# Kernel optimization log

Hardware: AMD Instinct MI355X
Metric: run time of the kernel (lower is better)

## Reference

```python
import jax, jax.numpy as jnp
import numpy as np

K = 5          # kernel_size
PAD = (K - 1) // 2  # fixed_padding with dilation=1, stride=1 -> 'same'


def setup_inputs() -> dict:
    key = jax.random.key(0)
    kx, kw = jax.random.split(key)
    x = jax.random.normal(kx, (4, 8, 512, 512), dtype=jnp.float32)
    # nn.Parameter initialized to zeros in the original; use small random values
    # so the op is non-trivial (math is identical for any weight values).
    weight = jax.random.normal(kw, (8, 8, K, K), dtype=jnp.float32) * 0.05
    return {"x": x, "weight": weight}


def reference(x, weight):
    """Morphological dilation2d with hard max (soft_max=False).

    out[n,o,h,w] = max_{c,dy,dx} ( x_pad[n,c,h+dy,w+dx] + weight[o,c,dy,dx] )
    Faithful to: pad zeros -> unfold -> weight + x -> max over dim C*k*k.
    Computed as a fused sliding-window max-plus reduction (no (N,C,k,k,H,W)
    unfold tensor is materialized; loop is over the fixed k*k kernel taps).
    """
    N, C, H, W = x.shape
    O = weight.shape[0]
    xp = jnp.pad(x, ((0, 0), (0, 0), (PAD, PAD), (PAD, PAD)))  # zero pad, as in F.pad
    out = jnp.full((N, O, H, W), -jnp.inf, dtype=x.dtype)
    for dy in range(K):
        for dx in range(K):
            patch = xp[:, :, dy:dy + H, dx:dx + W]           # (N,C,H,W)
            w_tap = weight[:, :, dy, dx]                      # (O,C)
            # (N,1,C,H,W) + (1,O,C,1,1) -> max over C -> (N,O,H,W)
            term = patch[:, None] + w_tap[None, :, :, None, None]
            out = jnp.maximum(out, jnp.max(term, axis=2))
    return out
```

## Files before the change

### kernel.cpp

```cpp
#include <hip/hip_runtime.h>
#include <math.h>
#include <stdint.h>

#define KK 5
#define PADK 2
#define C_IN 8
#define O_OUT 8
#define HH 512
#define WW 512
#define TH 8
#define TW 128
#define CH 4
#define LROWS 12
#define LCOLS 136
#define WSTR 12
#define NW (O_OUT * C_IN * KK * KK)
#define XHALF (CH * LROWS * (LCOLS / 2))

static __device__ __forceinline__ float max3f(float a, float b, float c) {
    float d;
    asm("v_max3_f32 %0, %1, %2, %3" : "=v"(d) : "v"(a), "v"(b), "v"(c));
    return d;
}

__global__ __launch_bounds__(512, 8)
void dil_kernel(const float* __restrict__ x,
                const float* __restrict__ wf,
                float* __restrict__ out) {
    __shared__ __align__(16) float xlds[CH][LROWS][LCOLS];
    __shared__ __align__(16) float wlds[C_IN * 4 * KK * WSTR];

    const int tid = threadIdx.x;
    const int w0 = blockIdx.x * TW;
    const int h0 = blockIdx.y * TH;
    const int n  = blockIdx.z;
    const float* xn = x + (size_t)n * (C_IN * HH * WW);

    const int l   = tid & 63;
    const int wid = tid >> 6;
    const int og  = wid & 3;
    const int rq  = wid >> 2;
    const int rbase = rq * 4;

    float acc[2][4][2];
    #pragma unroll
    for (int a = 0; a < 2; ++a)
        #pragma unroll
        for (int j = 0; j < 4; ++j) {
            acc[a][j][0] = -INFINITY;
            acc[a][j][1] = -INFINITY;
        }

    for (int h = 0; h < 2; ++h) {
        if (h) __syncthreads();

        for (int idx = tid; idx < XHALF; idx += 512) {
            int cc  = idx / (LROWS * (LCOLS / 2));
            int rem = idx - cc * (LROWS * (LCOLS / 2));
            int r   = rem / (LCOLS / 2);
            int jp  = rem - r * (LCOLS / 2);
            int gh = h0 - PADK + r;
            int gw = w0 - PADK + 2 * jp;
            float v0 = 0.f, v1 = 0.f;
            if ((unsigned)gh < (unsigned)HH) {
                const float* row = xn + ((size_t)(h * CH + cc) * HH + gh) * WW;
                if ((unsigned)gw < (unsigned)WW) v0 = row[gw];
                if ((unsigned)(gw + 1) < (unsigned)WW) v1 = row[gw + 1];
            }
            *(float2*)&xlds[cc][r][2 * jp] = make_float2(v0, v1);
        }
        if (h == 0) {
            for (int t = tid; t < NW; t += 512) {
                int dx = t % KK;  int q = t / KK;
                int o2 = q & 1;   q >>= 1;
                int dy = q % KK;  q /= KK;
                int g  = q & 3;   int c = q >> 2;
                int o = g * 2 + o2;
                wlds[((c * 4 + g) * KK + dy) * WSTR + o2 * KK + dx] =
                    wf[((o * C_IN + c) * KK + dy) * KK + dx];
            }
        }
        __syncthreads();

        for (int cc = 0; cc < CH; ++cc) {
            const float* wb = &wlds[((h * CH + cc) * 4 + og) * KK * WSTR];
            #pragma unroll
            for (int dy = 0; dy < KK; ++dy) {
                const float* wch = wb + dy * WSTR;
                float4 wa = *(const float4*)(wch);
                float4 wv = *(const float4*)(wch + 4);
                float2 wc2 = *(const float2*)(wch + 8);
                const float w[10] = {wa.x, wa.y, wa.z, wa.w,
                                     wv.x, wv.y, wv.z, wv.w, wc2.x, wc2.y};
                #pragma unroll
                for (int j = 0; j < 4; ++j) {
                    const float* lr = &xlds[cc][rbase + dy + j][2 * l];
                    float2 a = *(const float2*)(lr);
                    float2 b = *(const float2*)(lr + 2);
                    float2 d = *(const float2*)(lr + 4);
                    const float u0 = a.x, u1 = a.y, u2 = b.x,
                                u3 = b.y, u4 = d.x, u5 = d.y;
                    #pragma unroll
                    for (int o2 = 0; o2 < 2; ++o2) {
                        const float* wo = &w[o2 * 5];
                        float t0 = u0 + wo[0], t1 = u1 + wo[1],
                              t2 = u2 + wo[2], t3 = u3 + wo[3],
                              t4 = u4 + wo[4];
                        acc[o2][j][0] = max3f(acc[o2][j][0],
                                              max3f(t0, t1, t2),
                                              fmaxf(t3, t4));
                        float s0 = u1 + wo[0], s1 = u2 + wo[1],
                              s2 = u3 + wo[2], s3 = u4 + wo[3],
                              s4 = u5 + wo[4];
                        acc[o2][j][1] = max3f(acc[o2][j][1],
                                              max3f(s0, s1, s2),
                                              fmaxf(s3, s4));
                    }
                }
            }
        }
    }

    float* onp = out + (size_t)n * (O_OUT * HH * WW);
    const int hB = h0 + rbase;
    const int wcol = w0 + 2 * l;
    #pragma unroll
    for (int o2 = 0; o2 < 2; ++o2) {
        const int o = og * 2 + o2;
        #pragma unroll
        for (int j = 0; j < 4; ++j) {
            float2 rr = make_float2(acc[o2][j][0], acc[o2][j][1]);
            *(float2*)(&onp[((size_t)o * HH + hB + j) * WW + wcol]) = rr;
        }
    }
}

extern "C" void kernel_launch(void* const* d_in, const int* in_sizes, int n_in,
                              void* d_out, int out_size, void* d_ws, size_t ws_size,
                              hipStream_t stream) {
    const float* x   = (const float*)d_in[0];
    const float* wgt = (const float*)d_in[1];
    float* out = (float*)d_out;

    dim3 grid(WW / TW, HH / TH, 4);
    dim3 block(512);
    dil_kernel<<<grid, block, 0, stream>>>(x, wgt, out);
}
```

Measured before the change: 66.59 us.

## Remap warps to one row each computing all eight output channels

Each wavefront now owns one output row and accumulates all eight output channels, where before it owned four rows for two channels. Each loaded x window is reused across eight channels instead of two, cutting LDS reads of x per result. Weight loads from LDS rise, since each thread reads weights for all four channel groups per dy, though these reads are broadcast. The weight layout in LDS is reordered to match the new loop order.

```diff
diff --git a/kernel.cpp b/kernel.cpp
--- a/kernel.cpp
+++ b/kernel.cpp
@@ -28,7 +28,7 @@
                 const float* __restrict__ wf,
                 float* __restrict__ out) {
     __shared__ __align__(16) float xlds[CH][LROWS][LCOLS];
-    __shared__ __align__(16) float wlds[C_IN * 4 * KK * WSTR];
+    __shared__ __align__(16) float wlds[C_IN * KK * 4 * WSTR];
 
     const int tid = threadIdx.x;
     const int w0 = blockIdx.x * TW;
@@ -38,18 +38,13 @@
 
     const int l   = tid & 63;
     const int wid = tid >> 6;
-    const int og  = wid & 3;
-    const int rq  = wid >> 2;
-    const int rbase = rq * 4;
 
-    float acc[2][4][2];
+    float acc[O_OUT][2];
     #pragma unroll
-    for (int a = 0; a < 2; ++a)
-        #pragma unroll
-        for (int j = 0; j < 4; ++j) {
-            acc[a][j][0] = -INFINITY;
-            acc[a][j][1] = -INFINITY;
-        }
+    for (int o = 0; o < O_OUT; ++o) {
+        acc[o][0] = -INFINITY;
+        acc[o][1] = -INFINITY;
+    }
 
     for (int h = 0; h < 2; ++h) {
         if (h) __syncthreads();
@@ -76,45 +71,48 @@
                 int dy = q % KK;  q /= KK;
                 int g  = q & 3;   int c = q >> 2;
                 int o = g * 2 + o2;
-                wlds[((c * 4 + g) * KK + dy) * WSTR + o2 * KK + dx] =
+                wlds[((c * KK + dy) * 4 + g) * WSTR + o2 * KK + dx] =
                     wf[((o * C_IN + c) * KK + dy) * KK + dx];
             }
         }
         __syncthreads();
 
         for (int cc = 0; cc < CH; ++cc) {
-            const float* wb = &wlds[((h * CH + cc) * 4 + og) * KK * WSTR];
+            const int c = h * CH + cc;
             #pragma unroll
             for (int dy = 0; dy < KK; ++dy) {
-                const float* wch = wb + dy * WSTR;
-                float4 wa = *(const float4*)(wch);
-                float4 wv = *(const float4*)(wch + 4);
-                float2 wc2 = *(const float2*)(wch + 8);
-                const float w[10] = {wa.x, wa.y, wa.z, wa.w,
-                                     wv.x, wv.y, wv.z, wv.w, wc2.x, wc2.y};
+                const float* lr = &xlds[cc][wid + dy][2 * l];
+                float2 a = *(const float2*)(lr);
+                float2 b = *(const float2*)(lr + 2);
+                float2 d = *(const float2*)(lr + 4);
+                const float u0 = a.x, u1 = a.y, u2 = b.x,
+                            u3 = b.y, u4 = d.x, u5 = d.y;
+                const float* wdy = &wlds[(c * KK + dy) * 4 * WSTR];
                 #pragma unroll
-                for (int j = 0; j < 4; ++j) {
-                    const float* lr = &xlds[cc][rbase + dy + j][2 * l];
-                    float2 a = *(const float2*)(lr);
-                    float2 b = *(const float2*)(lr + 2);
-                    float2 d = *(const float2*)(lr + 4);
-                    const float u0 = a.x, u1 = a.y, u2 = b.x,
-                                u3 = b.y, u4 = d.x, u5 = d.y;
+                for (int g = 0; g < 4; ++g) {
+                    const float* wch = wdy + g * WSTR;
+                    float4 wa = *(const float4*)(wch);
+                    float4 wv = *(const float4*)(wch + 4);
+                    float2 wc2 = *(const float2*)(wch + 8);
+                    const float w[10] = {wa.x, wa.y, wa.z, wa.w,
+                                         wv.x, wv.y, wv.z, wv.w,
+                                         wc2.x, wc2.y};
                     #pragma unroll
                     for (int o2 = 0; o2 < 2; ++o2) {
+                        const int o = g * 2 + o2;
                         const float* wo = &w[o2 * 5];
                         float t0 = u0 + wo[0], t1 = u1 + wo[1],
                               t2 = u2 + wo[2], t3 = u3 + wo[3],
                               t4 = u4 + wo[4];
-                        acc[o2][j][0] = max3f(acc[o2][j][0],
-                                              max3f(t0, t1, t2),
-                                              fmaxf(t3, t4));
+                        acc[o][0] = max3f(acc[o][0],
+                                          max3f(t0, t1, t2),
+                                          fmaxf(t3, t4));
                         float s0 = u1 + wo[0], s1 = u2 + wo[1],
                               s2 = u3 + wo[2], s3 = u4 + wo[3],
                               s4 = u5 + wo[4];
-                        acc[o2][j][1] = max3f(acc[o2][j][1],
-                                              max3f(s0, s1, s2),
-                                              fmaxf(s3, s4));
+                        acc[o][1] = max3f(acc[o][1],
+                                          max3f(s0, s1, s2),
+                                          fmaxf(s3, s4));
                     }
                 }
             }
@@ -122,16 +120,12 @@
     }
 
     float* onp = out + (size_t)n * (O_OUT * HH * WW);
-    const int hB = h0 + rbase;
+    const int hB = h0 + wid;
     const int wcol = w0 + 2 * l;
     #pragma unroll
-    for (int o2 = 0; o2 < 2; ++o2) {
-        const int o = og * 2 + o2;
-        #pragma unroll
-        for (int j = 0; j < 4; ++j) {
-            float2 rr = make_float2(acc[o2][j][0], acc[o2][j][1]);
-            *(float2*)(&onp[((size_t)o * HH + hB + j) * WW + wcol]) = rr;
-        }
+    for (int o = 0; o < O_OUT; ++o) {
+        float2 rr = make_float2(acc[o][0], acc[o][1]);
+        *(float2*)(&onp[((size_t)o * HH + hB) * WW + wcol]) = rr;
     }
 }
 
```

Result: no change. 67.54 us (+1.4%).

## Prefetch second channel half into registers while computing first half

Applied to the files above, without the earlier changes.

Global loads of the input tile are staged through registers. The second channel-half is issued before computing the first half, so its memory latency overlaps the max-plus compute. Loads become unconditional, clamped float2 reads, with zero padding applied at LDS write time, which removes the branchy scalar loads. The cost is 14 extra VGPRs per thread under launch bounds of 512 threads with a minimum of 8 blocks per multiprocessor, which may cause spills or reduce occupancy.

```diff
diff --git a/kernel.cpp b/kernel.cpp
--- a/kernel.cpp
+++ b/kernel.cpp
@@ -16,6 +16,7 @@
 #define WSTR 12
 #define NW (O_OUT * C_IN * KK * KK)
 #define XHALF (CH * LROWS * (LCOLS / 2))
+#define NSTG 7
 
 static __device__ __forceinline__ float max3f(float a, float b, float c) {
     float d;
@@ -39,8 +40,49 @@
     const int l   = tid & 63;
     const int wid = tid >> 6;
     const int og  = wid & 3;
-    const int rq  = wid >> 2;
-    const int rbase = rq * 4;
+    const int rbase = (wid >> 2) * 4;
+
+    float2 stg[NSTG];
+
+    auto stageL = [&](int h) {
+        #pragma unroll
+        for (int k = 0; k < NSTG; ++k) {
+            int idx = tid + k * 512;
+            if (idx < XHALF) {
+                int cc  = idx / (LROWS * (LCOLS / 2));
+                int rem = idx - cc * (LROWS * (LCOLS / 2));
+                int r   = rem / (LCOLS / 2);
+                int jp  = rem - r * (LCOLS / 2);
+                int gh = h0 - PADK + r;
+                int gw = w0 - PADK + 2 * jp;
+                int ghc = min(max(gh, 0), HH - 1);
+                int gwc = min(max(gw, 0), WW - 2);
+                stg[k] = *(const float2*)(
+                    xn + ((size_t)(h * CH + cc) * HH + ghc) * WW + gwc);
+            }
+        }
+    };
+    auto stageW = [&]() {
+        float* base = &xlds[0][0][0];
+        #pragma unroll
+        for (int k = 0; k < NSTG; ++k) {
+            int idx = tid + k * 512;
+            if (idx < XHALF) {
+                int cc  = idx / (LROWS * (LCOLS / 2));
+                int rem = idx - cc * (LROWS * (LCOLS / 2));
+                int r   = rem / (LCOLS / 2);
+                int jp  = rem - r * (LCOLS / 2);
+                int gh = h0 - PADK + r;
+                int gw = w0 - PADK + 2 * jp;
+                bool ok = ((unsigned)gh < (unsigned)HH) &
+                          ((unsigned)gw < (unsigned)WW);
+                float2 v;
+                v.x = ok ? stg[k].x : 0.f;
+                v.y = ok ? stg[k].y : 0.f;
+                *(float2*)(base + 2 * idx) = v;
+            }
+        }
+    };
 
     float acc[2][4][2];
     #pragma unroll
@@ -51,37 +93,7 @@
             acc[a][j][1] = -INFINITY;
         }
 
-    for (int h = 0; h < 2; ++h) {
-        if (h) __syncthreads();
-
-        for (int idx = tid; idx < XHALF; idx += 512) {
-            int cc  = idx / (LROWS * (LCOLS / 2));
-            int rem = idx - cc * (LROWS * (LCOLS / 2));
-            int r   = rem / (LCOLS / 2);
-            int jp  = rem - r * (LCOLS / 2);
-            int gh = h0 - PADK + r;
-            int gw = w0 - PADK + 2 * jp;
-            float v0 = 0.f, v1 = 0.f;
-            if ((unsigned)gh < (unsigned)HH) {
-                const float* row = xn + ((size_t)(h * CH + cc) * HH + gh) * WW;
-                if ((unsigned)gw < (unsigned)WW) v0 = row[gw];
-                if ((unsigned)(gw + 1) < (unsigned)WW) v1 = row[gw + 1];
-            }
-            *(float2*)&xlds[cc][r][2 * jp] = make_float2(v0, v1);
-        }
-        if (h == 0) {
-            for (int t = tid; t < NW; t += 512) {
-                int dx = t % KK;  int q = t / KK;
-                int o2 = q & 1;   q >>= 1;
-                int dy = q % KK;  q /= KK;
-                int g  = q & 3;   int c = q >> 2;
-                int o = g * 2 + o2;
-                wlds[((c * 4 + g) * KK + dy) * WSTR + o2 * KK + dx] =
-                    wf[((o * C_IN + c) * KK + dy) * KK + dx];
-            }
-        }
-        __syncthreads();
-
+    auto compute = [&](int h) {
         for (int cc = 0; cc < CH; ++cc) {
             const float* wb = &wlds[((h * CH + cc) * 4 + og) * KK * WSTR];
             #pragma unroll
@@ -119,7 +131,28 @@
                 }
             }
         }
+    };
+
+    stageL(0);
+    for (int t = tid; t < NW; t += 512) {
+        int dx = t % KK;  int q = t / KK;
+        int o2 = q & 1;   q >>= 1;
+        int dy = q % KK;  q /= KK;
+        int g  = q & 3;   int c = q >> 2;
+        int o = g * 2 + o2;
+        wlds[((c * 4 + g) * KK + dy) * WSTR + o2 * KK + dx] =
+            wf[((o * C_IN + c) * KK + dy) * KK + dx];
     }
+    stageW();
+    __syncthreads();
+
+    stageL(1);
+    asm volatile("" ::: "memory");
+    compute(0);
+    __syncthreads();
+    stageW();
+    __syncthreads();
+    compute(1);
 
     float* onp = out + (size_t)n * (O_OUT * HH * WW);
     const int hB = h0 + rbase;
```

After: 75.80 us. +13.8%, slower.
